# Optimization experiments

Measured on AMD Instinct MI355X. Metric: run time of the kernel, lower is better.

## Reference

```python
import jax, jax.numpy as jnp
import numpy as np

B, N, C, H = 128, 256, 512, 2
HD = C // H  # head_dim == num_patches == N by construction of the module's einsums
ALPHA = 3.0


def _safe_pow(x, p):
    # x >= 0 (post-relu); avoid 0**p corner issues while matching x**p exactly for x>0
    pos = x > 0
    return jnp.where(pos, jnp.where(pos, x, 1.0) ** p, 0.0)


def setup_inputs() -> dict:
    key = jax.random.key(0)
    ks = jax.random.split(key, 12)
    s = 0.02
    return {
        "x": jax.random.normal(ks[0], (B, N, C), jnp.float32),
        "Wq": jax.random.normal(ks[1], (C, C), jnp.float32) * s,
        "bq": jnp.zeros((C,), jnp.float32),
        "Wk": jax.random.normal(ks[2], (C, C), jnp.float32) * s,
        "bk": jnp.zeros((C,), jnp.float32),
        "Wvs": jax.random.normal(ks[3], (C, C // 2), jnp.float32) * s,
        "bvs": jnp.zeros((C // 2,), jnp.float32),
        "Wvc": jax.random.normal(ks[4], (C, C // 2), jnp.float32) * s,
        "bvc": jnp.zeros((C // 2,), jnp.float32),
        "power": jnp.ones((1, H, 1, HD), jnp.float32),
        "W_s": jax.random.uniform(ks[5], (N, HD // 2), jnp.float32),
        "W_c": jax.random.uniform(ks[6], (N, HD // 2), jnp.float32),
        "Wp": jax.random.normal(ks[7], (C, C), jnp.float32) * s,
        "bp": jnp.zeros((C,), jnp.float32),
    }


def reference(x, Wq, bq, Wk, bk, Wvs, bvs, Wvc, bvc, power, W_s, W_c, Wp, bp):
    b, n, c = x.shape
    h, hd = H, c // H
    # projections -> [B, H, N, hd] (or hd//2 for values)
    q = (x @ Wq + bq).reshape(b, n, h, hd).transpose(0, 2, 1, 3)
    k = (x @ Wk + bk).reshape(b, n, h, hd).transpose(0, 2, 1, 3)
    v_s = (x @ Wvs + bvs).reshape(b, n, h, hd // 2).transpose(0, 2, 1, 3)
    v_c = (x @ Wvc + bvc).reshape(b, n, h, hd // 2).transpose(0, 2, 1, 3)

    power_val = 1.0 + ALPHA * jax.nn.sigmoid(power)  # [1,H,1,hd]
    q_pos = _safe_pow(jax.nn.relu(q), power_val)
    q_neg = _safe_pow(jax.nn.relu(-q), power_val)
    k_pos = _safe_pow(jax.nn.relu(k), power_val)
    k_neg = _safe_pow(jax.nn.relu(-k), power_val)

    # kv_s = einsum(k_pos,v_s)+einsum(k_neg,v_s) == einsum(k_pos+k_neg, v_s); same for kv_c
    k_abs = k_pos + k_neg
    q_abs = q_pos + q_neg
    kv_s = jnp.einsum('bhnj,bhjd->bhnd', k_abs, v_s)
    q_s_context = jnp.einsum('bhni,bhid->bhnd', q_abs, kv_s)
    kv_c = jnp.einsum('bhnj,bhjd->bhnd', k_abs, v_c)
    q_c_context = jnp.einsum('bhni,bhid->bhnd', q_abs, kv_c)

    kp_sum = k_pos.sum(-1)  # [B,H,N]
    kn_sum = k_neg.sum(-1)
    denom_s = jnp.einsum('bhni,bhi->bhn', q_pos, kp_sum) + jnp.einsum('bhni,bhi->bhn', q_neg, kn_sum)
    denom_c = jnp.einsum('bhni,bhi->bhn', q_pos, kn_sum) + jnp.einsum('bhni,bhi->bhn', q_neg, kp_sum)

    attn_s = q_s_context / (denom_s[..., None] + 1e-6) * W_s  # W_s: [N, hd//2]
    attn_c = q_c_context / (denom_c[..., None] + 1e-6) * W_c

    out = jnp.concatenate([attn_s, attn_c], axis=-1)  # [B,H,N,hd]
    out = out.transpose(0, 2, 1, 3).reshape(b, n, c)
    return out @ Wp + bp
```

## Files before the change

### kernel.cpp

```cpp
#include <hip/hip_runtime.h>
#include <hip/hip_bf16.h>
#include <math.h>

typedef unsigned int u32;
typedef short bf16x8 __attribute__((ext_vector_type(8)));
typedef float f32x4 __attribute__((ext_vector_type(4)));
typedef u32 u32x4 __attribute__((ext_vector_type(4)));

__device__ __forceinline__ float bf2f(short s) {
    u32 u = ((u32)(unsigned short)s) << 16;
    return __builtin_bit_cast(float, u);
}
__device__ __forceinline__ short f2bf(float f) {
    u32 u = __builtin_bit_cast(u32, f);
    u32 r = u + 0x7fffu + ((u >> 16) & 1u);
    return (short)(r >> 16);
}
__device__ __forceinline__ float fast_log2(float x) {
    float r; asm volatile("v_log_f32 %0, %1" : "=v"(r) : "v"(x)); return r;
}
__device__ __forceinline__ float fast_exp2(float x) {
    float r; asm volatile("v_exp_f32 %0, %1" : "=v"(r) : "v"(x)); return r;
}
__device__ __forceinline__ void gload_lds16(const short* g, short* lds) {
    __builtin_amdgcn_global_load_lds(
        (const __attribute__((address_space(1))) u32*)g,
        (__attribute__((address_space(3))) u32*)lds, 16, 0, 0);
}
__device__ __forceinline__ bf16x8 stripsign(bf16x8 v) {
    u32x4 u = __builtin_bit_cast(u32x4, v);
    u &= 0x7fff7fffu;
    return __builtin_bit_cast(bf16x8, u);
}

struct P {
    const float* bcat; const float* pcol;
    short* qa; short* ka;
    short* vt; short* kvt;
    const float* dsb; const float* dcb; const float* Ws; const float* Wc;
    short* Y; float* out;
};

__global__ void k_pack(const float* __restrict__ Wq, const float* __restrict__ Wk,
                       const float* __restrict__ Wvs, const float* __restrict__ Wvc,
                       const float* __restrict__ Wp,
                       const float* __restrict__ bq, const float* __restrict__ bk,
                       const float* __restrict__ bvs, const float* __restrict__ bvc,
                       const float* __restrict__ bp, const float* __restrict__ power,
                       short* __restrict__ WcatT, float* __restrict__ bcat, float* __restrict__ pcol)
{
    int i = blockIdx.x * 256 + threadIdx.x;
    int r = i >> 9, k = i & 511;
    float w;
    if (r < 512)       w = Wq[k * 512 + r];
    else if (r < 1024) w = Wk[k * 512 + (r - 512)];
    else if (r < 1536) {
        int rr = r - 1024; int h = rr >> 8; int d = rr & 255;
        w = (d < 128) ? Wvs[k * 256 + h * 128 + d] : Wvc[k * 256 + h * 128 + (d - 128)];
    } else             w = Wp[k * 512 + (r - 1536)];
    WcatT[i] = f2bf(w);

    if (i < 2048) {
        float bb;
        if (i < 512)       bb = bq[i];
        else if (i < 1024) bb = bk[i - 512];
        else if (i < 1536) {
            int rr = i - 1024; int h = rr >> 8; int d = rr & 255;
            bb = (d < 128) ? bvs[h * 128 + d] : bvc[h * 128 + (d - 128)];
        } else             bb = bp[i - 1536];
        bcat[i] = bb;
    }
    if (i < 512) pcol[i] = 1.0f + 3.0f / (1.0f + expf(-power[i]));
}

__global__ void k_cast(const float* __restrict__ x, short* __restrict__ xb)
{
    int i = blockIdx.x * 256 + threadIdx.x;
    float4 v = ((const float4*)x)[i];
    short4 s;
    s.x = f2bf(v.x); s.y = f2bf(v.y); s.z = f2bf(v.z); s.w = f2bf(v.w);
    ((short4*)xb)[i] = s;
}

__global__ void k_ksum(const short* __restrict__ ka,
                       float* __restrict__ kpsum, float* __restrict__ knsum)
{
    int gid = blockIdx.x * 256 + threadIdx.x;
    int gw = gid >> 6;
    int lane = gid & 63;
    short4 a4 = ((const short4*)(ka + ((size_t)gw << 8)))[lane];
    short aa[4] = {a4.x, a4.y, a4.z, a4.w};
    float sp = 0.f, sn = 0.f;
#pragma unroll
    for (int j = 0; j < 4; ++j) {
        float a = fabsf(bf2f(aa[j]));
        if (((unsigned short)aa[j] >> 15) == 0) sp += a; else sn += a;
    }
#pragma unroll
    for (int m = 1; m < 64; m <<= 1) { sp += __shfl_xor(sp, m, 64); sn += __shfl_xor(sn, m, 64); }
    if (lane == 0) { kpsum[gw] = sp; knsum[gw] = sn; }
}

__global__ void k_denom(const short* __restrict__ qa,
                        const float* __restrict__ kpsum, const float* __restrict__ knsum,
                        float* __restrict__ dsb, float* __restrict__ dcb)
{
    int gid = blockIdx.x * 256 + threadIdx.x;
    int gw = gid >> 6;
    int lane = gid & 63;
    int bhl = gw >> 8;
    short4 q4 = ((const short4*)(qa + ((size_t)gw << 8)))[lane];
    float4 kp4 = ((const float4*)(kpsum + ((size_t)bhl << 8)))[lane];
    float4 kn4 = ((const float4*)(knsum + ((size_t)bhl << 8)))[lane];
    short qq[4] = {q4.x, q4.y, q4.z, q4.w};
    float kp[4] = {kp4.x, kp4.y, kp4.z, kp4.w};
    float kn[4] = {kn4.x, kn4.y, kn4.z, kn4.w};
    float ss = 0.f, sc = 0.f;
#pragma unroll
    for (int j = 0; j < 4; ++j) {
        float a = fabsf(bf2f(qq[j]));
        if (((unsigned short)qq[j] >> 15) == 0) { ss += a * kp[j]; sc += a * kn[j]; }
        else                                    { ss += a * kn[j]; sc += a * kp[j]; }
    }
#pragma unroll
    for (int m = 1; m < 64; m <<= 1) { ss += __shfl_xor(ss, m, 64); sc += __shfl_xor(sc, m, 64); }
    if (lane == 0) { dsb[gw] = ss; dcb[gw] = sc; }
}

#define MODE_QK  0
#define MODE_VT  1
#define MODE_KV  2
#define MODE_CTX 3
#define MODE_OUT 4

template <int MODE>
__launch_bounds__(256, 4)
__global__ void gemm_nt(const short* __restrict__ Ag, const short* __restrict__ Bg,
                        int K, int tilesN, P p)
{
    __shared__ __align__(16) short sm[16384];
    short* As = sm;
    short* Bs = sm + 8192;

    const int nwg = gridDim.x * gridDim.y;
    const int s = blockIdx.y * gridDim.x + blockIdx.x;
    const int cpx = nwg >> 3;
    const int lin = (s & 7) * cpx + (s >> 3);

    int tm, tn, bhl;
    if (MODE == MODE_KV || MODE == MODE_CTX) {
        bhl = lin >> 2;
        int rem = lin & 3;
        tm = rem / tilesN; tn = rem % tilesN;
    } else {
        bhl = 0;
        tm = lin / tilesN; tn = lin % tilesN;
    }

    const short* A = Ag;
    const short* B = Bg;
    if (MODE == MODE_KV || MODE == MODE_CTX) {
        A += (size_t)bhl << 16;
        B += (size_t)bhl << 16;
    }
    constexpr bool stripA = (MODE == MODE_CTX);
    constexpr bool stripB = (MODE == MODE_KV);

    const int t = threadIdx.x;
    const int lane = t & 63;
    const int w = t >> 6;
    const int wr = w >> 1, wc = w & 1;

    f32x4 acc[4][4];
#pragma unroll
    for (int i = 0; i < 4; ++i)
#pragma unroll
        for (int j = 0; j < 4; ++j) acc[i][j] = 0.f;

    const int nkt = K >> 6;
    for (int kt = 0; kt < nkt; ++kt) {
#pragma unroll
        for (int q4i = 0; q4i < 4; ++q4i) {
            int seg = w * 4 + q4i;
            int r = seg * 8 + (lane >> 3);
            int c = (lane & 7) ^ (r & 7);
            gload_lds16(A + (size_t)(tm * 128 + r) * K + kt * 64 + c * 8, &As[seg * 512]);
            gload_lds16(B + (size_t)(tn * 128 + r) * K + kt * 64 + c * 8, &Bs[seg * 512]);
        }
        __syncthreads();
#pragma unroll
        for (int kk = 0; kk < 2; ++kk) {
            bf16x8 af[4], bfr[4];
#pragma unroll
            for (int mt = 0; mt < 4; ++mt) {
                int row = wr * 64 + mt * 16 + (lane & 15);
                int ch = kk * 4 + (lane >> 4);
                af[mt] = *(const bf16x8*)(&As[row * 64 + ((ch ^ (row & 7)) << 3)]);
                if constexpr (stripA) af[mt] = stripsign(af[mt]);
            }
#pragma unroll
            for (int nt = 0; nt < 4; ++nt) {
                int row = wc * 64 + nt * 16 + (lane & 15);
                int ch = kk * 4 + (lane >> 4);
                bfr[nt] = *(const bf16x8*)(&Bs[row * 64 + ((ch ^ (row & 7)) << 3)]);
                if constexpr (stripB) bfr[nt] = stripsign(bfr[nt]);
            }
#pragma unroll
            for (int mt = 0; mt < 4; ++mt)
#pragma unroll
                for (int nt = 0; nt < 4; ++nt)
                    acc[mt][nt] = __builtin_amdgcn_mfma_f32_16x16x32_bf16(af[mt], bfr[nt], acc[mt][nt], 0, 0, 0);
        }
        __syncthreads();
    }

    if (MODE == MODE_QK || MODE == MODE_VT) {
#pragma unroll
        for (int mt = 0; mt < 4; ++mt) {
#pragma unroll
            for (int nt = 0; nt < 4; ++nt) {
#pragma unroll
                for (int r = 0; r < 4; ++r) {
                    int lrow = wr * 64 + mt * 16 + (lane >> 4) * 4 + r;
                    int lcol = wc * 64 + nt * 16 + (lane & 15);
                    float v = acc[mt][nt][r];
                    short sv;
                    if (MODE == MODE_QK) {
                        int col_g = tn * 128 + lcol;
                        v += p.bcat[col_g];
                        float pw = p.pcol[col_g & 511];
                        float a = (v != 0.0f) ? fast_exp2(pw * fast_log2(fabsf(v))) : 0.0f;
                        unsigned short sa = (unsigned short)f2bf(a);
                        sa |= (unsigned short)((__builtin_bit_cast(u32, v) >> 16) & 0x8000u);
                        sv = (short)sa;
                    } else {
                        v += p.bcat[1024 + tm * 128 + lrow];
                        sv = f2bf(v);
                    }
                    int g = lcol >> 3;
                    sm[lrow * 128 + ((g ^ (lrow & 7)) << 3) + (lcol & 7)] = sv;
                }
            }
        }
        __syncthreads();
#pragma unroll
        for (int i = 0; i < 8; ++i) {
            int slot = i * 256 + t;
            int lrow = slot >> 4;
            int g = slot & 15;
            bf16x8 val = *(const bf16x8*)&sm[lrow * 128 + ((g ^ (lrow & 7)) << 3)];
            if (MODE == MODE_QK) {
                int row_g = tm * 128 + lrow;
                int col0 = tn * 128 + g * 8;
                int bl = row_g >> 8, n = row_g & 255;
                int h = (col0 >> 8) & 1;
                short* dst = (col0 < 512) ? p.qa : p.ka;
                *(bf16x8*)(dst + (((size_t)((bl * 2 + h) * 256 + n)) << 8) + (col0 & 255)) = val;
            } else {
                int d_g = tm * 128 + lrow;
                int col0 = tn * 128 + g * 8;
                int h = d_g >> 8, d = d_g & 255;
                int bl = col0 >> 8, n0 = col0 & 255;
                *(bf16x8*)(p.vt + (((size_t)((bl * 2 + h) * 256 + d)) << 8) + n0) = val;
            }
        }
    } else if (MODE == MODE_OUT) {
        float* smf = (float*)sm;
#pragma unroll
        for (int half = 0; half < 2; ++half) {
            if (wr == half) {
#pragma unroll
                for (int mt = 0; mt < 4; ++mt) {
#pragma unroll
                    for (int nt = 0; nt < 4; ++nt) {
#pragma unroll
                        for (int r = 0; r < 4; ++r) {
                            int lrow = mt * 16 + (lane >> 4) * 4 + r;
                            int lcol = wc * 64 + nt * 16 + (lane & 15);
                            float v = acc[mt][nt][r] + p.bcat[1536 + tn * 128 + lcol];
                            int g = lcol >> 2;
                            smf[lrow * 128 + ((g ^ (lrow & 7)) << 2) + (lcol & 3)] = v;
                        }
                    }
                }
            }
            __syncthreads();
#pragma unroll
            for (int i = 0; i < 8; ++i) {
                int slot = i * 256 + t;
                int lrow = slot >> 5;
                int g = slot & 31;
                float4 val = *(const float4*)&smf[lrow * 128 + ((g ^ (lrow & 7)) << 2)];
                int row_g = tm * 128 + half * 64 + lrow;
                *(float4*)(p.out + ((size_t)row_g << 9) + tn * 128 + g * 4) = val;
            }
            __syncthreads();
        }
    } else {
#pragma unroll
        for (int mt = 0; mt < 4; ++mt) {
#pragma unroll
            for (int nt = 0; nt < 4; ++nt) {
#pragma unroll
                for (int r = 0; r < 4; ++r) {
                    int row = tm * 128 + wr * 64 + mt * 16 + (lane >> 4) * 4 + r;
                    int col = tn * 128 + wc * 64 + nt * 16 + (lane & 15);
                    float v = acc[mt][nt][r];
                    if (MODE == MODE_KV) {
                        p.kvt[((size_t)bhl << 16) + (row << 8) + col] = f2bf(v);
                    } else {
                        int n = row, d = col;
                        float den = ((d < 128) ? p.dsb : p.dcb)[bhl * 256 + n] + 1e-6f;
                        float wgt = (d < 128) ? p.Ws[n * 128 + d] : p.Wc[n * 128 + (d - 128)];
                        v = v / den * wgt;
                        int bl = bhl >> 1, h = bhl & 1;
                        p.Y[((size_t)(bl * 256 + n) << 9) + h * 256 + d] = f2bf(v);
                    }
                }
            }
        }
    }
}

extern "C" void kernel_launch(void* const* d_in, const int* in_sizes, int n_in,
                              void* d_out, int out_size, void* d_ws, size_t ws_size,
                              hipStream_t stream)
{
    const float* x     = (const float*)d_in[0];
    const float* Wq    = (const float*)d_in[1];
    const float* bq    = (const float*)d_in[2];
    const float* Wk    = (const float*)d_in[3];
    const float* bk    = (const float*)d_in[4];
    const float* Wvs   = (const float*)d_in[5];
    const float* bvs   = (const float*)d_in[6];
    const float* Wvc   = (const float*)d_in[7];
    const float* bvc   = (const float*)d_in[8];
    const float* power = (const float*)d_in[9];
    const float* Ws    = (const float*)d_in[10];
    const float* Wc    = (const float*)d_in[11];
    const float* Wp    = (const float*)d_in[12];
    const float* bp    = (const float*)d_in[13];
    (void)in_sizes; (void)n_in; (void)out_size; (void)ws_size;

    char* ws = (char*)d_ws;
    size_t off = 0;
    auto alloc = [&](size_t bytes) { void* pp = ws + off; off += (bytes + 255) & ~(size_t)255; return pp; };
    short* Wcat = (short*)alloc(2097152);
    float* bcat = (float*)alloc(8192);
    float* pcol = (float*)alloc(2048);
    short* xb   = (short*)alloc(33554432);
    short* qa   = (short*)alloc(33554432);
    short* ka   = (short*)alloc(33554432);
    short* vt   = (short*)alloc(33554432);
    short* kvt  = (short*)alloc(33554432);
    float* kpsum= (float*)alloc(262144);
    float* knsum= (float*)alloc(262144);
    float* dsb  = (float*)alloc(262144);
    float* dcb  = (float*)alloc(262144);

    P p{};
    p.bcat = bcat; p.pcol = pcol;
    p.qa = qa; p.ka = ka;
    p.vt = vt; p.kvt = kvt;
    p.dsb = dsb; p.dcb = dcb; p.Ws = Ws; p.Wc = Wc;
    p.Y = xb; p.out = nullptr;

    k_pack<<<4096, 256, 0, stream>>>(Wq, Wk, Wvs, Wvc, Wp, bq, bk, bvs, bvc, bp, power, Wcat, bcat, pcol);

    k_cast<<<16384, 256, 0, stream>>>(x, xb);

    gemm_nt<MODE_QK><<<dim3(2048, 1), 256, 0, stream>>>(xb, Wcat, 512, 8, p);

    gemm_nt<MODE_VT><<<dim3(1024, 1), 256, 0, stream>>>(Wcat + 1024 * 512, xb, 512, 256, p);

    gemm_nt<MODE_KV><<<dim3(4, 256), 256, 0, stream>>>(vt, ka, 256, 2, p);

    k_ksum<<<16384, 256, 0, stream>>>(ka, kpsum, knsum);
    k_denom<<<16384, 256, 0, stream>>>(qa, kpsum, knsum, dsb, dcb);

    gemm_nt<MODE_CTX><<<dim3(4, 256), 256, 0, stream>>>(qa, kvt, 256, 2, p);

    P po = p;
    po.out = (float*)d_out;
    gemm_nt<MODE_OUT><<<dim3(1024, 1), 256, 0, stream>>>(xb, Wcat + 1536 * 512, 512, 4, po);
}
```

Measured before the change: 207.3 us.

## Fuse k-sum and denominator reductions into KV and CTX GEMM kernels

Removes the separate k_ksum and k_denom kernels. The KV GEMM now computes the positive and negative row sums of k from its LDS tiles, and the CTX GEMM computes the denominators from its q tiles plus those k sums staged in shared memory. This saves two full passes over the 32 MB qa and ka buffers and two kernel launches. In exchange it adds an extra __syncthreads per k-iteration, scalar reduction work inside the GEMM loops, and the denominator is recomputed redundantly by each column tile.

```diff
diff --git a/kernel.cpp b/kernel.cpp
--- a/kernel.cpp
+++ b/kernel.cpp
@@ -37,7 +37,8 @@
     const float* bcat; const float* pcol;
     short* qa; short* ka;
     short* vt; short* kvt;
-    const float* dsb; const float* dcb; const float* Ws; const float* Wc;
+    float* kpsum; float* knsum;
+    const float* Ws; const float* Wc;
     short* Y; float* out;
 };
 
@@ -82,51 +83,6 @@
     ((short4*)xb)[i] = s;
 }
 
-__global__ void k_ksum(const short* __restrict__ ka,
-                       float* __restrict__ kpsum, float* __restrict__ knsum)
-{
-    int gid = blockIdx.x * 256 + threadIdx.x;
-    int gw = gid >> 6;
-    int lane = gid & 63;
-    short4 a4 = ((const short4*)(ka + ((size_t)gw << 8)))[lane];
-    short aa[4] = {a4.x, a4.y, a4.z, a4.w};
-    float sp = 0.f, sn = 0.f;
-#pragma unroll
-    for (int j = 0; j < 4; ++j) {
-        float a = fabsf(bf2f(aa[j]));
-        if (((unsigned short)aa[j] >> 15) == 0) sp += a; else sn += a;
-    }
-#pragma unroll
-    for (int m = 1; m < 64; m <<= 1) { sp += __shfl_xor(sp, m, 64); sn += __shfl_xor(sn, m, 64); }
-    if (lane == 0) { kpsum[gw] = sp; knsum[gw] = sn; }
-}
-
-__global__ void k_denom(const short* __restrict__ qa,
-                        const float* __restrict__ kpsum, const float* __restrict__ knsum,
-                        float* __restrict__ dsb, float* __restrict__ dcb)
-{
-    int gid = blockIdx.x * 256 + threadIdx.x;
-    int gw = gid >> 6;
-    int lane = gid & 63;
-    int bhl = gw >> 8;
-    short4 q4 = ((const short4*)(qa + ((size_t)gw << 8)))[lane];
-    float4 kp4 = ((const float4*)(kpsum + ((size_t)bhl << 8)))[lane];
-    float4 kn4 = ((const float4*)(knsum + ((size_t)bhl << 8)))[lane];
-    short qq[4] = {q4.x, q4.y, q4.z, q4.w};
-    float kp[4] = {kp4.x, kp4.y, kp4.z, kp4.w};
-    float kn[4] = {kn4.x, kn4.y, kn4.z, kn4.w};
-    float ss = 0.f, sc = 0.f;
-#pragma unroll
-    for (int j = 0; j < 4; ++j) {
-        float a = fabsf(bf2f(qq[j]));
-        if (((unsigned short)qq[j] >> 15) == 0) { ss += a * kp[j]; sc += a * kn[j]; }
-        else                                    { ss += a * kn[j]; sc += a * kp[j]; }
-    }
-#pragma unroll
-    for (int m = 1; m < 64; m <<= 1) { ss += __shfl_xor(ss, m, 64); sc += __shfl_xor(sc, m, 64); }
-    if (lane == 0) { dsb[gw] = ss; dcb[gw] = sc; }
-}
-
 #define MODE_QK  0
 #define MODE_VT  1
 #define MODE_KV  2
@@ -139,6 +95,7 @@
                         int K, int tilesN, P p)
 {
     __shared__ __align__(16) short sm[16384];
+    __shared__ __align__(16) float wls[256];
     short* As = sm;
     short* Bs = sm + 8192;
 
@@ -177,6 +134,10 @@
 #pragma unroll
         for (int j = 0; j < 4; ++j) acc[i][j] = 0.f;
 
+    float ksp = 0.f, ksn = 0.f;
+    float dds = 0.f, ddc = 0.f;
+    const int rrow = t >> 1, sub = t & 1;
+
     const int nkt = K >> 6;
     for (int kt = 0; kt < nkt; ++kt) {
 #pragma unroll
@@ -187,7 +148,44 @@
             gload_lds16(A + (size_t)(tm * 128 + r) * K + kt * 64 + c * 8, &As[seg * 512]);
             gload_lds16(B + (size_t)(tn * 128 + r) * K + kt * 64 + c * 8, &Bs[seg * 512]);
         }
+        if constexpr (MODE == MODE_CTX) {
+            if (t < 32) {
+                const float* src = (t < 16) ? p.kpsum : p.knsum;
+                int idx = bhl * 256 + kt * 64 + (t & 15) * 4;
+                *(float4*)&wls[(t < 16 ? 0 : 64) + (t & 15) * 4] = *(const float4*)&src[idx];
+            }
+        }
         __syncthreads();
+
+        if constexpr (MODE == MODE_KV) {
+#pragma unroll
+            for (int cl = 0; cl < 4; ++cl) {
+                int c = sub * 4 + cl;
+                bf16x8 vv = *(const bf16x8*)&Bs[rrow * 64 + ((c ^ (rrow & 7)) << 3)];
+#pragma unroll
+                for (int e = 0; e < 8; ++e) {
+                    short sv = vv[e];
+                    float a = fabsf(bf2f(sv));
+                    if (((unsigned short)sv >> 15) == 0) ksp += a; else ksn += a;
+                }
+            }
+        }
+        if constexpr (MODE == MODE_CTX) {
+#pragma unroll
+            for (int cl = 0; cl < 4; ++cl) {
+                int c = sub * 4 + cl;
+                bf16x8 vv = *(const bf16x8*)&As[rrow * 64 + ((c ^ (rrow & 7)) << 3)];
+#pragma unroll
+                for (int e = 0; e < 8; ++e) {
+                    short sv = vv[e];
+                    float a = fabsf(bf2f(sv));
+                    float kp = wls[c * 8 + e], kn = wls[64 + c * 8 + e];
+                    if (((unsigned short)sv >> 15) == 0) { dds += a * kp; ddc += a * kn; }
+                    else                                 { dds += a * kn; ddc += a * kp; }
+                }
+            }
+        }
+
 #pragma unroll
         for (int kk = 0; kk < 2; ++kk) {
             bf16x8 af[4], bfr[4];
@@ -211,6 +209,23 @@
                 for (int nt = 0; nt < 4; ++nt)
                     acc[mt][nt] = __builtin_amdgcn_mfma_f32_16x16x32_bf16(af[mt], bfr[nt], acc[mt][nt], 0, 0, 0);
         }
+        __syncthreads();
+    }
+
+    if constexpr (MODE == MODE_KV) {
+        ksp += __shfl_xor(ksp, 1, 64);
+        ksn += __shfl_xor(ksn, 1, 64);
+        if (tm == 0 && sub == 0) {
+            p.kpsum[bhl * 256 + tn * 128 + rrow] = ksp;
+            p.knsum[bhl * 256 + tn * 128 + rrow] = ksn;
+        }
+    }
+    float* dsb_l = wls;
+    float* dcb_l = wls + 128;
+    if constexpr (MODE == MODE_CTX) {
+        dds += __shfl_xor(dds, 1, 64);
+        ddc += __shfl_xor(ddc, 1, 64);
+        if (sub == 0) { dsb_l[rrow] = dds; dcb_l[rrow] = ddc; }
         __syncthreads();
     }
 
@@ -303,14 +318,15 @@
             for (int nt = 0; nt < 4; ++nt) {
 #pragma unroll
                 for (int r = 0; r < 4; ++r) {
-                    int row = tm * 128 + wr * 64 + mt * 16 + (lane >> 4) * 4 + r;
+                    int lr = wr * 64 + mt * 16 + (lane >> 4) * 4 + r;
+                    int row = tm * 128 + lr;
                     int col = tn * 128 + wc * 64 + nt * 16 + (lane & 15);
                     float v = acc[mt][nt][r];
                     if (MODE == MODE_KV) {
                         p.kvt[((size_t)bhl << 16) + (row << 8) + col] = f2bf(v);
                     } else {
                         int n = row, d = col;
-                        float den = ((d < 128) ? p.dsb : p.dcb)[bhl * 256 + n] + 1e-6f;
+                        float den = ((d < 128) ? dsb_l : dcb_l)[lr] + 1e-6f;
                         float wgt = (d < 128) ? p.Ws[n * 128 + d] : p.Wc[n * 128 + (d - 128)];
                         v = v / den * wgt;
                         int bl = bhl >> 1, h = bhl & 1;
@@ -355,14 +371,13 @@
     short* kvt  = (short*)alloc(33554432);
     float* kpsum= (float*)alloc(262144);
     float* knsum= (float*)alloc(262144);
-    float* dsb  = (float*)alloc(262144);
-    float* dcb  = (float*)alloc(262144);
 
     P p{};
     p.bcat = bcat; p.pcol = pcol;
     p.qa = qa; p.ka = ka;
     p.vt = vt; p.kvt = kvt;
-    p.dsb = dsb; p.dcb = dcb; p.Ws = Ws; p.Wc = Wc;
+    p.kpsum = kpsum; p.knsum = knsum;
+    p.Ws = Ws; p.Wc = Wc;
     p.Y = xb; p.out = nullptr;
 
     k_pack<<<4096, 256, 0, stream>>>(Wq, Wk, Wvs, Wvc, Wp, bq, bk, bvs, bvc, bp, power, Wcat, bcat, pcol);
@@ -374,9 +389,6 @@
     gemm_nt<MODE_VT><<<dim3(1024, 1), 256, 0, stream>>>(Wcat + 1024 * 512, xb, 512, 256, p);
 
     gemm_nt<MODE_KV><<<dim3(4, 256), 256, 0, stream>>>(vt, ka, 256, 2, p);
-
-    k_ksum<<<16384, 256, 0, stream>>>(ka, kpsum, knsum);
-    k_denom<<<16384, 256, 0, stream>>>(qa, kpsum, knsum, dsb, dcb);
 
     gemm_nt<MODE_CTX><<<dim3(4, 256), 256, 0, stream>>>(qa, kvt, 256, 2, p);
 
```

Measured after the change: 235.1 us. 13.4% more time.
